# Performance work log

Measured on AMD Instinct MI355X. Metric: run time of the kernel, lower is better.

Reference implementation:

```python
import jax, jax.numpy as jnp
import numpy as np

R, S, C, HID = 8192, 128, 32, 64   # rays, samples/ray, grid_chn, mlp_hidden_chn
G = 128                            # voxel grid resolution
COLOR_CHN = 3
NUM_HARM = 3
OPACITY_INIT_BIAS = -5.0
GAIN = 1.0
HE_DIM = 3 * 2 * NUM_HARM + 3      # harmonic embedding dim = 21

def _relu(x):
    return jnp.maximum(x, 0.0)

def _trilinear(grid, p):
    # grid: [G, G, G, Cg] indexed [z, y, x]; p: [N, 3] xyz coords in [-1, 1]
    g = grid.shape[0]
    c = (p + 1.0) * 0.5 * (g - 1)  # align_corners=True convention
    c0f = jnp.floor(c)
    fr = c - c0f
    c0 = jnp.clip(c0f.astype(jnp.int32), 0, g - 1)
    c1 = jnp.clip(c0 + 1, 0, g - 1)
    x0, y0, z0 = c0[:, 0], c0[:, 1], c0[:, 2]
    x1, y1, z1 = c1[:, 0], c1[:, 1], c1[:, 2]
    fx, fy, fz = fr[:, 0:1], fr[:, 1:2], fr[:, 2:3]
    out = jnp.zeros((p.shape[0], grid.shape[-1]), grid.dtype)
    for xi, wx in ((x0, 1.0 - fx), (x1, fx)):
        for yi, wy in ((y0, 1.0 - fy), (y1, fy)):
            for zi, wz in ((z0, 1.0 - fz), (z1, fz)):
                out = out + (wx * wy * wz) * grid[zi, yi, xi]
    return out

def _harmonic(d):
    # [sin(2^i d), cos(2^i d)] for i<NUM_HARM, with raw direction appended
    freqs = 2.0 ** jnp.arange(NUM_HARM, dtype=jnp.float32)
    ang = d[:, None, :] * freqs[None, :, None]  # [R, NH, 3]
    n = d.shape[0]
    return jnp.concatenate([jnp.sin(ang).reshape(n, -1), jnp.cos(ang).reshape(n, -1), d], axis=-1)

def _forward(origins, directions, near, far, feature_grid, Wr, br, Wt1, bt1, Wt2, bt2, Wo1, bo1, Wo2, bo2, Wc1, bc1, Wc2, bc2):
    n_rays = origins.shape[0]
    # stratified midpoints between near and far
    t = near[:, None] + (far - near)[:, None] * (jnp.arange(S, dtype=jnp.float32) + 0.5) / S
    pts = origins[:, None, :] + t[..., None] * directions[:, None, :]  # [R, S, 3]
    feats = _trilinear(feature_grid, pts.reshape(-1, 3)).reshape(n_rays, S, -1)
    # trunk MLP
    e = _relu(feats @ Wt1 + bt1)
    e = _relu(e @ Wt2 + bt2)
    # opacity MLP (last-layer bias carries opacity_init_bias)
    raw = _relu(e @ Wo1 + bo1) @ Wo2 + bo2  # [R, S, 1]
    density = jax.nn.softplus(GAIN * raw[..., 0])
    delta = ((far - near) / S)[:, None]
    alpha = 1.0 - jnp.exp(-delta * density)  # [R, S]
    trans = jnp.cumprod(1.0 - alpha, axis=1)
    T = jnp.concatenate([jnp.ones((n_rays, 1), alpha.dtype), trans[:, :-1]], axis=1)
    w = T * alpha  # compositing weights
    # color branch: harmonic ray-direction encoding added to color-MLP input
    ray_enc = _harmonic(directions) @ Wr + br  # [R, HID]
    cin = e + ray_enc[:, None, :]
    col = jax.nn.sigmoid(_relu(cin @ Wc1 + bc1) @ Wc2 + bc2)  # [R, S, COLOR_CHN]
    color = jnp.einsum('rs,rsc->rc', w, col)
    mask = 1.0 - trans[:, -1]
    color = color + (1.0 - mask)[:, None] * 0.0  # bg_color = 0.0
    return color, mask

def setup_inputs():
    key = jax.random.key(0)
    ks = jax.random.split(key, 16)
    directions = jax.random.normal(ks[0], (R, 3), jnp.float32)
    directions = directions / jnp.linalg.norm(directions, axis=-1, keepdims=True)
    origins = jnp.zeros((R, 3), jnp.float32)
    near = jnp.full((R,), 0.1, jnp.float32)
    far = jnp.full((R,), 1.0, jnp.float32)
    feature_grid = jax.random.normal(ks[1], (G, G, G, C), jnp.float32) * 0.1
    def lin(k, i, o):
        s = (2.0 / (i + o)) ** 0.5
        return jax.random.normal(k, (i, o), jnp.float32) * s
    return {
        'origins': origins, 'directions': directions, 'near': near, 'far': far,
        'feature_grid': feature_grid,
        'Wr': lin(ks[2], HE_DIM, HID), 'br': jnp.zeros((HID,), jnp.float32),
        'Wt1': lin(ks[3], C, HID), 'bt1': jnp.zeros((HID,), jnp.float32),
        'Wt2': lin(ks[4], HID, HID), 'bt2': jnp.zeros((HID,), jnp.float32),
        'Wo1': lin(ks[5], HID, HID), 'bo1': jnp.zeros((HID,), jnp.float32),
        'Wo2': lin(ks[6], HID, 1), 'bo2': jnp.full((1,), OPACITY_INIT_BIAS, jnp.float32),
        'Wc1': lin(ks[7], HID, HID), 'bc1': jnp.zeros((HID,), jnp.float32),
        'Wc2': lin(ks[8], HID, COLOR_CHN), 'bc2': jnp.zeros((COLOR_CHN,), jnp.float32),
    }

def reference(origins, directions, near, far, feature_grid, Wr, br, Wt1, bt1, Wt2, bt2, Wo1, bo1, Wo2, bo2, Wc1, bc1, Wc2, bc2):
    return _forward(origins, directions, near, far, feature_grid, Wr, br, Wt1, bt1, Wt2, bt2, Wo1, bo1, Wo2, bo2, Wc1, bc1, Wc2, bc2)
```

## Files before the change

### kernel.cpp

```cpp
#include <hip/hip_runtime.h>
#include <math.h>

#define NRAYS 8192
#define XPAD 72

typedef short s16x8 __attribute__((ext_vector_type(8)));
typedef float f32x4 __attribute__((ext_vector_type(4)));

__device__ __forceinline__ unsigned short f2bf(float x){
  unsigned u = __float_as_uint(x);
  u += 0x7FFF + ((u >> 16) & 1);
  return (unsigned short)(u >> 16);
}
__device__ __forceinline__ float bf2f(unsigned short s){ return __uint_as_float(((unsigned)s) << 16); }
__device__ __forceinline__ float softplusf_(float x){ return (x > 20.f) ? x : log1pf(expf(x)); }
__device__ __forceinline__ float sigmoidf_(float x){ return 1.f / (1.f + expf(-x)); }

__global__ void prep_weights(const float* __restrict__ Wt1, const float* __restrict__ Wt2,
                             const float* __restrict__ Wo1, const float* __restrict__ Wc1,
                             unsigned short* __restrict__ ws)
{
  const int i0 = blockIdx.x * blockDim.x + threadIdx.x;
  const int st = gridDim.x * blockDim.x;
  for (int i = i0; i < 2048; i += st){ int n = i >> 5, k = i & 31; ws[i]         = f2bf(Wt1[k * 64 + n]); }
  for (int i = i0; i < 4096; i += st){ int n = i >> 6, k = i & 63; ws[2048 + i]  = f2bf(Wt2[k * 64 + n]); }
  for (int i = i0; i < 4096; i += st){ int n = i >> 6, k = i & 63; ws[6144 + i]  = f2bf(Wo1[k * 64 + n]); }
  for (int i = i0; i < 4096; i += st){ int n = i >> 6, k = i & 63; ws[10240 + i] = f2bf(Wc1[k * 64 + n]); }
}

__device__ __forceinline__ void layer64(const s16x8 a[4][2], const unsigned short* __restrict__ wt,
                                        const float* __restrict__ bias, int ln15, int quad,
                                        f32x4 acc[4][4])
{
  float bv[4];
#pragma unroll
  for (int nt = 0; nt < 4; ++nt) bv[nt] = bias[nt * 16 + ln15];
#pragma unroll
  for (int mt = 0; mt < 4; ++mt)
#pragma unroll
    for (int nt = 0; nt < 4; ++nt){ f32x4 c; c[0] = bv[nt]; c[1] = bv[nt]; c[2] = bv[nt]; c[3] = bv[nt]; acc[mt][nt] = c; }
#pragma unroll
  for (int ks = 0; ks < 2; ++ks){
    s16x8 b[4];
#pragma unroll
    for (int nt = 0; nt < 4; ++nt)
      b[nt] = *(const s16x8*)(wt + (nt * 16 + ln15) * 64 + ks * 32 + quad * 8);
#pragma unroll
    for (int mt = 0; mt < 4; ++mt)
#pragma unroll
      for (int nt = 0; nt < 4; ++nt)
        acc[mt][nt] = __builtin_amdgcn_mfma_f32_16x16x32_bf16(a[mt][ks], b[nt], acc[mt][nt], 0, 0, 0);
  }
}

__device__ __forceinline__ void store_relu(unsigned short* __restrict__ sX, int wrow, int ln15, int quad,
                                           const f32x4 acc[4][4])
{
#pragma unroll
  for (int mt = 0; mt < 4; ++mt){
    const int rowb = wrow + mt * 16 + quad * 4;
#pragma unroll
    for (int nt = 0; nt < 4; ++nt){
      const int col = nt * 16 + ln15;
#pragma unroll
      for (int r = 0; r < 4; ++r)
        sX[(rowb + r) * XPAD + col] = f2bf(fmaxf(acc[mt][nt][r], 0.f));
    }
  }
}

extern "C" __global__ __launch_bounds__(256, 2)
void lightplane_fwd(const float* __restrict__ origins, const float* __restrict__ dirs,
                    const float* __restrict__ nearv,   const float* __restrict__ farv,
                    const float* __restrict__ grid,
                    const float* __restrict__ Wr,  const float* __restrict__ br,
                    const float* __restrict__ bt1, const float* __restrict__ bt2,
                    const float* __restrict__ bo1,
                    const float* __restrict__ Wo2, const float* __restrict__ bo2,
                    const float* __restrict__ bc1,
                    const float* __restrict__ Wc2, const float* __restrict__ bc2,
                    const unsigned short* __restrict__ ws,
                    float* __restrict__ out)
{
  __shared__ unsigned short s_X[256 * XPAD];
  __shared__ float s_scan[2][128];
  __shared__ float s_enc[2][64];
  __shared__ float s_part[2][2][4];

  const int tid   = threadIdx.x;
  const int lane  = tid & 63;
  const int wv    = tid >> 6;
  const int ln15  = lane & 15, quad = lane >> 4;
  const int wrow  = wv * 64;
  const int r_loc = tid >> 7;
  const int s_idx = tid & 127;
  const int ray   = blockIdx.x * 2 + r_loc;

  if (tid < 128) {
    const int rr = tid >> 6, j = tid & 63;
    const int rg = blockIdx.x * 2 + rr;
    const float ddx = dirs[rg * 3 + 0], ddy = dirs[rg * 3 + 1], ddz = dirs[rg * 3 + 2];
    float h[21]; float f = 1.f;
#pragma unroll
    for (int q = 0; q < 3; ++q) {
      h[q * 3 + 0] = sinf(ddx * f); h[q * 3 + 1] = sinf(ddy * f); h[q * 3 + 2] = sinf(ddz * f);
      h[9 + q * 3 + 0] = cosf(ddx * f); h[9 + q * 3 + 1] = cosf(ddy * f); h[9 + q * 3 + 2] = cosf(ddz * f);
      f *= 2.f;
    }
    h[18] = ddx; h[19] = ddy; h[20] = ddz;
    float a = br[j];
#pragma unroll
    for (int i = 0; i < 21; ++i) a = fmaf(h[i], Wr[i * 64 + j], a);
    s_enc[rr][j] = a;
  }

  const float dx = dirs[ray * 3 + 0], dy = dirs[ray * 3 + 1], dz = dirs[ray * 3 + 2];
  const float ox = origins[ray * 3 + 0], oy = origins[ray * 3 + 1], oz = origins[ray * 3 + 2];
  const float nr = nearv[ray], fa = farv[ray];
  const float t  = nr + (fa - nr) * ((s_idx + 0.5f) * (1.0f / 128.0f));
  const float px = fmaf(t, dx, ox), py = fmaf(t, dy, oy), pz = fmaf(t, dz, oz);

  const float cx = (px + 1.f) * 63.5f, cy = (py + 1.f) * 63.5f, cz = (pz + 1.f) * 63.5f;
  const float fx0 = floorf(cx), fy0 = floorf(cy), fz0 = floorf(cz);
  const float frx = cx - fx0, fry = cy - fy0, frz = cz - fz0;
  int ix0 = min(max((int)fx0, 0), 127), iy0 = min(max((int)fy0, 0), 127), iz0 = min(max((int)fz0, 0), 127);
  int ix1 = min(ix0 + 1, 127), iy1 = min(iy0 + 1, 127), iz1 = min(iz0 + 1, 127);
  const float wxs[2] = {1.f - frx, frx}, wys[2] = {1.f - fry, fry}, wzs[2] = {1.f - frz, frz};
  const int xi[2] = {ix0, ix1}, yi[2] = {iy0, iy1}, zi[2] = {iz0, iz1};

  float fe[32];
#pragma unroll
  for (int k = 0; k < 32; ++k) fe[k] = 0.f;
#pragma unroll
  for (int a = 0; a < 2; ++a)
#pragma unroll
    for (int b2 = 0; b2 < 2; ++b2)
#pragma unroll
      for (int c2 = 0; c2 < 2; ++c2) {
        const float wgt = wzs[a] * wys[b2] * wxs[c2];
        const float4* g4 = (const float4*)(grid + ((size_t)((zi[a] * 128 + yi[b2]) * 128 + xi[c2])) * 32);
#pragma unroll
        for (int k = 0; k < 8; ++k) {
          float4 g = g4[k];
          fe[4 * k + 0] = fmaf(wgt, g.x, fe[4 * k + 0]);
          fe[4 * k + 1] = fmaf(wgt, g.y, fe[4 * k + 1]);
          fe[4 * k + 2] = fmaf(wgt, g.z, fe[4 * k + 2]);
          fe[4 * k + 3] = fmaf(wgt, g.w, fe[4 * k + 3]);
        }
      }

#pragma unroll
  for (int q = 0; q < 4; ++q) {
    s16x8 v;
#pragma unroll
    for (int j = 0; j < 8; ++j) v[j] = (short)f2bf(fe[q * 8 + j]);
    *(s16x8*)&s_X[tid * XPAD + q * 8] = v;
  }

  f32x4 acc[4][4];

  {
    s16x8 a1[4];
#pragma unroll
    for (int mt = 0; mt < 4; ++mt)
      a1[mt] = *(const s16x8*)&s_X[(wrow + mt * 16 + ln15) * XPAD + quad * 8];
    float bv[4];
#pragma unroll
    for (int nt = 0; nt < 4; ++nt) bv[nt] = bt1[nt * 16 + ln15];
#pragma unroll
    for (int mt = 0; mt < 4; ++mt)
#pragma unroll
      for (int nt = 0; nt < 4; ++nt){ f32x4 c; c[0]=bv[nt];c[1]=bv[nt];c[2]=bv[nt];c[3]=bv[nt]; acc[mt][nt]=c; }
    s16x8 b[4];
#pragma unroll
    for (int nt = 0; nt < 4; ++nt)
      b[nt] = *(const s16x8*)(ws + (nt * 16 + ln15) * 32 + quad * 8);
#pragma unroll
    for (int mt = 0; mt < 4; ++mt)
#pragma unroll
      for (int nt = 0; nt < 4; ++nt)
        acc[mt][nt] = __builtin_amdgcn_mfma_f32_16x16x32_bf16(a1[mt], b[nt], acc[mt][nt], 0, 0, 0);
    store_relu(s_X, wrow, ln15, quad, acc);
  }

  {
    s16x8 a[4][2];
#pragma unroll
    for (int ks = 0; ks < 2; ++ks)
#pragma unroll
      for (int mt = 0; mt < 4; ++mt)
        a[mt][ks] = *(const s16x8*)&s_X[(wrow + mt * 16 + ln15) * XPAD + ks * 32 + quad * 8];
    layer64(a, ws + 2048, bt2, ln15, quad, acc);
    store_relu(s_X, wrow, ln15, quad, acc);
  }

  s16x8 ea[4][2];
#pragma unroll
  for (int ks = 0; ks < 2; ++ks)
#pragma unroll
    for (int mt = 0; mt < 4; ++mt)
      ea[mt][ks] = *(const s16x8*)&s_X[(wrow + mt * 16 + ln15) * XPAD + ks * 32 + quad * 8];

  layer64(ea, ws + 6144, bo1, ln15, quad, acc);
  store_relu(s_X, wrow, ln15, quad, acc);
  float raw = bo2[0];
#pragma unroll
  for (int q = 0; q < 8; ++q) {
    s16x8 v = *(const s16x8*)&s_X[tid * XPAD + q * 8];
#pragma unroll
    for (int j = 0; j < 8; ++j)
      raw = fmaf(bf2f((unsigned short)v[j]), Wo2[q * 8 + j], raw);
  }
  const float density = softplusf_(raw);
  const float delta   = (fa - nr) * (1.0f / 128.0f);
  const float alpha   = 1.f - expf(-delta * density);

  __syncthreads();

  {
    s16x8 a[4][2];
#pragma unroll
    for (int ks = 0; ks < 2; ++ks) {
      const float* ep = &s_enc[r_loc][ks * 32 + quad * 8];
      float4 e0 = *(const float4*)ep;
      float4 e1 = *(const float4*)(ep + 4);
      float encv[8] = {e0.x, e0.y, e0.z, e0.w, e1.x, e1.y, e1.z, e1.w};
#pragma unroll
      for (int mt = 0; mt < 4; ++mt) {
        s16x8 v;
#pragma unroll
        for (int j = 0; j < 8; ++j)
          v[j] = (short)f2bf(bf2f((unsigned short)ea[mt][ks][j]) + encv[j]);
        a[mt][ks] = v;
      }
    }
    layer64(a, ws + 10240, bc1, ln15, quad, acc);
    store_relu(s_X, wrow, ln15, quad, acc);
  }
  float c0 = bc2[0], c1 = bc2[1], c2 = bc2[2];
#pragma unroll
  for (int q = 0; q < 8; ++q) {
    s16x8 v = *(const s16x8*)&s_X[tid * XPAD + q * 8];
#pragma unroll
    for (int j = 0; j < 8; ++j) {
      const float h = bf2f((unsigned short)v[j]);
      c0 = fmaf(h, Wc2[(q * 8 + j) * 3 + 0], c0);
      c1 = fmaf(h, Wc2[(q * 8 + j) * 3 + 1], c1);
      c2 = fmaf(h, Wc2[(q * 8 + j) * 3 + 2], c2);
    }
  }
  c0 = sigmoidf_(c0); c1 = sigmoidf_(c1); c2 = sigmoidf_(c2);

  float vv = 1.f - alpha;
  s_scan[r_loc][s_idx] = vv;
  __syncthreads();
#pragma unroll
  for (int off = 1; off < 128; off <<= 1) {
    const float u = (s_idx >= off) ? s_scan[r_loc][s_idx - off] : 1.f;
    __syncthreads();
    vv *= u;
    s_scan[r_loc][s_idx] = vv;
    __syncthreads();
  }
  const float Texcl = (s_idx == 0) ? 1.f : s_scan[r_loc][s_idx - 1];
  const float wgt = Texcl * alpha;

  float p0 = wgt * c0, p1 = wgt * c1, p2 = wgt * c2;
#pragma unroll
  for (int off = 32; off > 0; off >>= 1) {
    p0 += __shfl_down(p0, off, 64);
    p1 += __shfl_down(p1, off, 64);
    p2 += __shfl_down(p2, off, 64);
  }
  if ((tid & 63) == 0) {
    const int wvi = s_idx >> 6;
    s_part[r_loc][wvi][0] = p0; s_part[r_loc][wvi][1] = p1; s_part[r_loc][wvi][2] = p2;
  }
  __syncthreads();
  if (s_idx == 0) {
    out[ray * 3 + 0] = s_part[r_loc][0][0] + s_part[r_loc][1][0];
    out[ray * 3 + 1] = s_part[r_loc][0][1] + s_part[r_loc][1][1];
    out[ray * 3 + 2] = s_part[r_loc][0][2] + s_part[r_loc][1][2];
    out[NRAYS * 3 + ray] = 1.f - s_scan[r_loc][127];
  }
}

extern "C" void kernel_launch(void* const* d_in, const int* in_sizes, int n_in,
                              void* d_out, int out_size, void* d_ws, size_t ws_size,
                              hipStream_t stream)
{
  (void)in_sizes; (void)n_in; (void)out_size; (void)ws_size;
  const float* origins = (const float*)d_in[0];
  const float* dirs    = (const float*)d_in[1];
  const float* nearv   = (const float*)d_in[2];
  const float* farv    = (const float*)d_in[3];
  const float* grid    = (const float*)d_in[4];
  const float* Wr  = (const float*)d_in[5];
  const float* br  = (const float*)d_in[6];
  const float* Wt1 = (const float*)d_in[7];
  const float* bt1 = (const float*)d_in[8];
  const float* Wt2 = (const float*)d_in[9];
  const float* bt2 = (const float*)d_in[10];
  const float* Wo1 = (const float*)d_in[11];
  const float* bo1 = (const float*)d_in[12];
  const float* Wo2 = (const float*)d_in[13];
  const float* bo2 = (const float*)d_in[14];
  const float* Wc1 = (const float*)d_in[15];
  const float* bc1 = (const float*)d_in[16];
  const float* Wc2 = (const float*)d_in[17];
  const float* bc2 = (const float*)d_in[18];
  unsigned short* ws = (unsigned short*)d_ws;
  float* out = (float*)d_out;

  prep_weights<<<16, 256, 0, stream>>>(Wt1, Wt2, Wo1, Wc1, ws);
  lightplane_fwd<<<NRAYS / 2, 256, 0, stream>>>(origins, dirs, nearv, farv, grid,
                                                Wr, br, bt1, bt2, bo1, Wo2, bo2,
                                                bc1, Wc2, bc2, ws, out);
}
```

Baseline: 507.9 us.

## Transpose MFMA layout, fuse output heads in registers, use wave-level transmittance scan

The MLP is restructured so the bf16 weights become the MFMA A operand and the per-sample activations become B. Activations stay in small per-wave LDS scratch tiles instead of one shared 256-row buffer. The opacity and color final layers are reduced directly from MFMA accumulators with cross-lane shuffles, which removes the LDS round trips for the last hidden layers. The 128-step block-wide cumulative-product scan, with its many __syncthreads, is replaced by a 64-lane shuffle scan plus a two-wave combine, and launch bounds now allow 4 blocks per SM. In exchange, trunk layer 2 is computed twice (once with the encoding added for the color branch, once without) and register pressure rises under the tighter occupancy bound.

```diff
diff --git a/kernel.cpp b/kernel.cpp
--- a/kernel.cpp
+++ b/kernel.cpp
@@ -1,18 +1,22 @@
 #include <hip/hip_runtime.h>
+#include <hip/hip_bf16.h>
 #include <math.h>
 
 #define NRAYS 8192
-#define XPAD 72
 
 typedef short s16x8 __attribute__((ext_vector_type(8)));
 typedef float f32x4 __attribute__((ext_vector_type(4)));
 
+__device__ __forceinline__ unsigned pk2(float a, float b){
+  union { __hip_bfloat162 h; unsigned u; } cv;
+  cv.h = __float22bfloat162_rn(make_float2(a, b));
+  return cv.u;
+}
 __device__ __forceinline__ unsigned short f2bf(float x){
   unsigned u = __float_as_uint(x);
   u += 0x7FFF + ((u >> 16) & 1);
   return (unsigned short)(u >> 16);
 }
-__device__ __forceinline__ float bf2f(unsigned short s){ return __uint_as_float(((unsigned)s) << 16); }
 __device__ __forceinline__ float softplusf_(float x){ return (x > 20.f) ? x : log1pf(expf(x)); }
 __device__ __forceinline__ float sigmoidf_(float x){ return 1.f / (1.f + expf(-x)); }
 
@@ -28,48 +32,7 @@
   for (int i = i0; i < 4096; i += st){ int n = i >> 6, k = i & 63; ws[10240 + i] = f2bf(Wc1[k * 64 + n]); }
 }
 
-__device__ __forceinline__ void layer64(const s16x8 a[4][2], const unsigned short* __restrict__ wt,
-                                        const float* __restrict__ bias, int ln15, int quad,
-                                        f32x4 acc[4][4])
-{
-  float bv[4];
-#pragma unroll
-  for (int nt = 0; nt < 4; ++nt) bv[nt] = bias[nt * 16 + ln15];
-#pragma unroll
-  for (int mt = 0; mt < 4; ++mt)
-#pragma unroll
-    for (int nt = 0; nt < 4; ++nt){ f32x4 c; c[0] = bv[nt]; c[1] = bv[nt]; c[2] = bv[nt]; c[3] = bv[nt]; acc[mt][nt] = c; }
-#pragma unroll
-  for (int ks = 0; ks < 2; ++ks){
-    s16x8 b[4];
-#pragma unroll
-    for (int nt = 0; nt < 4; ++nt)
-      b[nt] = *(const s16x8*)(wt + (nt * 16 + ln15) * 64 + ks * 32 + quad * 8);
-#pragma unroll
-    for (int mt = 0; mt < 4; ++mt)
-#pragma unroll
-      for (int nt = 0; nt < 4; ++nt)
-        acc[mt][nt] = __builtin_amdgcn_mfma_f32_16x16x32_bf16(a[mt][ks], b[nt], acc[mt][nt], 0, 0, 0);
-  }
-}
-
-__device__ __forceinline__ void store_relu(unsigned short* __restrict__ sX, int wrow, int ln15, int quad,
-                                           const f32x4 acc[4][4])
-{
-#pragma unroll
-  for (int mt = 0; mt < 4; ++mt){
-    const int rowb = wrow + mt * 16 + quad * 4;
-#pragma unroll
-    for (int nt = 0; nt < 4; ++nt){
-      const int col = nt * 16 + ln15;
-#pragma unroll
-      for (int r = 0; r < 4; ++r)
-        sX[(rowb + r) * XPAD + col] = f2bf(fmaxf(acc[mt][nt][r], 0.f));
-    }
-  }
-}
-
-extern "C" __global__ __launch_bounds__(256, 2)
+extern "C" __global__ __launch_bounds__(256, 4)
 void lightplane_fwd(const float* __restrict__ origins, const float* __restrict__ dirs,
                     const float* __restrict__ nearv,   const float* __restrict__ farv,
                     const float* __restrict__ grid,
@@ -82,19 +45,21 @@
                     const unsigned short* __restrict__ ws,
                     float* __restrict__ out)
 {
-  __shared__ unsigned short s_X[256 * XPAD];
-  __shared__ float s_scan[2][128];
+  __shared__ float s_scr[4 * 2304];
   __shared__ float s_enc[2][64];
-  __shared__ float s_part[2][2][4];
-
-  const int tid   = threadIdx.x;
-  const int lane  = tid & 63;
-  const int wv    = tid >> 6;
-  const int ln15  = lane & 15, quad = lane >> 4;
-  const int wrow  = wv * 64;
-  const int r_loc = tid >> 7;
-  const int s_idx = tid & 127;
-  const int ray   = blockIdx.x * 2 + r_loc;
+  __shared__ float s_wtot[2][2];
+  __shared__ float s_part[2][2][3];
+
+  const int tid  = threadIdx.x;
+  const int lane = tid & 63, wv = tid >> 6;
+  const int ln15 = lane & 15, quad = lane >> 4;
+  const int r_loc = wv >> 1, hh = wv & 1;
+  const int ray  = blockIdx.x * 2 + r_loc;
+  const int s_idx = hh * 64 + lane;
+
+  float*          wbase = s_scr + wv * 2304;
+  unsigned*       uscr  = (unsigned*)wbase;
+  unsigned short* fscr  = (unsigned short*)wbase;
 
   if (tid < 128) {
     const int rr = tid >> 6, j = tid & 63;
@@ -134,11 +99,11 @@
 #pragma unroll
   for (int a = 0; a < 2; ++a)
 #pragma unroll
-    for (int b2 = 0; b2 < 2; ++b2)
+    for (int b2i = 0; b2i < 2; ++b2i)
 #pragma unroll
       for (int c2 = 0; c2 < 2; ++c2) {
-        const float wgt = wzs[a] * wys[b2] * wxs[c2];
-        const float4* g4 = (const float4*)(grid + ((size_t)((zi[a] * 128 + yi[b2]) * 128 + xi[c2])) * 32);
+        const float wgt = wzs[a] * wys[b2i] * wxs[c2];
+        const float4* g4 = (const float4*)(grid + ((size_t)((zi[a] * 128 + yi[b2i]) * 128 + xi[c2])) * 32);
 #pragma unroll
         for (int k = 0; k < 8; ++k) {
           float4 g = g4[k];
@@ -149,139 +114,208 @@
         }
       }
 
-#pragma unroll
-  for (int q = 0; q < 4; ++q) {
-    s16x8 v;
-#pragma unroll
-    for (int j = 0; j < 8; ++j) v[j] = (short)f2bf(fe[q * 8 + j]);
-    *(s16x8*)&s_X[tid * XPAD + q * 8] = v;
-  }
-
-  f32x4 acc[4][4];
-
   {
-    s16x8 a1[4];
-#pragma unroll
-    for (int mt = 0; mt < 4; ++mt)
-      a1[mt] = *(const s16x8*)&s_X[(wrow + mt * 16 + ln15) * XPAD + quad * 8];
-    float bv[4];
-#pragma unroll
-    for (int nt = 0; nt < 4; ++nt) bv[nt] = bt1[nt * 16 + ln15];
-#pragma unroll
-    for (int mt = 0; mt < 4; ++mt)
-#pragma unroll
-      for (int nt = 0; nt < 4; ++nt){ f32x4 c; c[0]=bv[nt];c[1]=bv[nt];c[2]=bv[nt];c[3]=bv[nt]; acc[mt][nt]=c; }
-    s16x8 b[4];
-#pragma unroll
-    for (int nt = 0; nt < 4; ++nt)
-      b[nt] = *(const s16x8*)(ws + (nt * 16 + ln15) * 32 + quad * 8);
-#pragma unroll
-    for (int mt = 0; mt < 4; ++mt)
+    unsigned* frow = uscr + lane * 20;
+#pragma unroll
+    for (int q = 0; q < 4; ++q) {
+      uint4 v;
+      v.x = pk2(fe[8 * q + 0], fe[8 * q + 1]); v.y = pk2(fe[8 * q + 2], fe[8 * q + 3]);
+      v.z = pk2(fe[8 * q + 4], fe[8 * q + 5]); v.w = pk2(fe[8 * q + 6], fe[8 * q + 7]);
+      *(uint4*)(frow + 4 * q) = v;
+    }
+  }
+  __syncthreads();
+
+  s16x8 b1[4];
+#pragma unroll
+  for (int nt = 0; nt < 4; ++nt)
+    b1[nt] = *(const s16x8*)(fscr + (16 * nt + ln15) * 40 + quad * 8);
+
+#pragma unroll
+  for (int mt = 0; mt < 4; ++mt) {
+    s16x8 a1 = *(const s16x8*)(ws + (16 * mt + ln15) * 32 + quad * 8);
+    float4 bb = *(const float4*)(bt1 + 16 * mt + 4 * quad);
+    f32x4 acc[4];
+#pragma unroll
+    for (int nt = 0; nt < 4; ++nt) {
+      f32x4 c; c[0] = bb.x; c[1] = bb.y; c[2] = bb.z; c[3] = bb.w;
+      acc[nt] = __builtin_amdgcn_mfma_f32_16x16x32_bf16(a1, b1[nt], c, 0, 0, 0);
+    }
+#pragma unroll
+    for (int nt = 0; nt < 4; ++nt) {
+      uint2 p;
+      p.x = pk2(fmaxf(acc[nt][0], 0.f), fmaxf(acc[nt][1], 0.f));
+      p.y = pk2(fmaxf(acc[nt][2], 0.f), fmaxf(acc[nt][3], 0.f));
+      *(uint2*)(uscr + (16 * nt + ln15) * 36 + 8 * mt + 2 * quad) = p;
+    }
+  }
+  s16x8 b2[4][2];
+#pragma unroll
+  for (int nt = 0; nt < 4; ++nt)
+#pragma unroll
+    for (int ks = 0; ks < 2; ++ks)
+      b2[nt][ks] = *(const s16x8*)(uscr + (16 * nt + ln15) * 36 + 16 * ks + 4 * quad);
+
+#pragma unroll
+  for (int mt = 0; mt < 4; ++mt) {
+    float4 bb = *(const float4*)(bt2 + 16 * mt + 4 * quad);
+    f32x4 acc[4];
+#pragma unroll
+    for (int nt = 0; nt < 4; ++nt) { f32x4 c; c[0]=bb.x;c[1]=bb.y;c[2]=bb.z;c[3]=bb.w; acc[nt]=c; }
+#pragma unroll
+    for (int ks = 0; ks < 2; ++ks) {
+      s16x8 a = *(const s16x8*)(ws + 2048 + (16 * mt + ln15) * 64 + ks * 32 + quad * 8);
 #pragma unroll
       for (int nt = 0; nt < 4; ++nt)
-        acc[mt][nt] = __builtin_amdgcn_mfma_f32_16x16x32_bf16(a1[mt], b[nt], acc[mt][nt], 0, 0, 0);
-    store_relu(s_X, wrow, ln15, quad, acc);
-  }
-
-  {
-    s16x8 a[4][2];
+        acc[nt] = __builtin_amdgcn_mfma_f32_16x16x32_bf16(a, b2[nt][ks], acc[nt], 0, 0, 0);
+    }
+    float4 en = *(const float4*)(&s_enc[r_loc][16 * mt + 4 * quad]);
+#pragma unroll
+    for (int nt = 0; nt < 4; ++nt) {
+      uint2 p;
+      p.x = pk2(fmaxf(acc[nt][0], 0.f) + en.x, fmaxf(acc[nt][1], 0.f) + en.y);
+      p.y = pk2(fmaxf(acc[nt][2], 0.f) + en.z, fmaxf(acc[nt][3], 0.f) + en.w);
+      *(uint2*)(uscr + (16 * nt + ln15) * 36 + 8 * mt + 2 * quad) = p;
+    }
+  }
+  s16x8 b4[4][2];
+#pragma unroll
+  for (int nt = 0; nt < 4; ++nt)
 #pragma unroll
     for (int ks = 0; ks < 2; ++ks)
-#pragma unroll
-      for (int mt = 0; mt < 4; ++mt)
-        a[mt][ks] = *(const s16x8*)&s_X[(wrow + mt * 16 + ln15) * XPAD + ks * 32 + quad * 8];
-    layer64(a, ws + 2048, bt2, ln15, quad, acc);
-    store_relu(s_X, wrow, ln15, quad, acc);
-  }
-
-  s16x8 ea[4][2];
-#pragma unroll
-  for (int ks = 0; ks < 2; ++ks)
-#pragma unroll
-    for (int mt = 0; mt < 4; ++mt)
-      ea[mt][ks] = *(const s16x8*)&s_X[(wrow + mt * 16 + ln15) * XPAD + ks * 32 + quad * 8];
-
-  layer64(ea, ws + 6144, bo1, ln15, quad, acc);
-  store_relu(s_X, wrow, ln15, quad, acc);
-  float raw = bo2[0];
-#pragma unroll
-  for (int q = 0; q < 8; ++q) {
-    s16x8 v = *(const s16x8*)&s_X[tid * XPAD + q * 8];
-#pragma unroll
-    for (int j = 0; j < 8; ++j)
-      raw = fmaf(bf2f((unsigned short)v[j]), Wo2[q * 8 + j], raw);
-  }
-  const float density = softplusf_(raw);
-  const float delta   = (fa - nr) * (1.0f / 128.0f);
-  const float alpha   = 1.f - expf(-delta * density);
-
+      b4[nt][ks] = *(const s16x8*)(uscr + (16 * nt + ln15) * 36 + 16 * ks + 4 * quad);
+
+#pragma unroll
+  for (int mt = 0; mt < 4; ++mt) {
+    float4 bb = *(const float4*)(bt2 + 16 * mt + 4 * quad);
+    f32x4 acc[4];
+#pragma unroll
+    for (int nt = 0; nt < 4; ++nt) { f32x4 c; c[0]=bb.x;c[1]=bb.y;c[2]=bb.z;c[3]=bb.w; acc[nt]=c; }
+#pragma unroll
+    for (int ks = 0; ks < 2; ++ks) {
+      s16x8 a = *(const s16x8*)(ws + 2048 + (16 * mt + ln15) * 64 + ks * 32 + quad * 8);
+#pragma unroll
+      for (int nt = 0; nt < 4; ++nt)
+        acc[nt] = __builtin_amdgcn_mfma_f32_16x16x32_bf16(a, b2[nt][ks], acc[nt], 0, 0, 0);
+    }
+#pragma unroll
+    for (int nt = 0; nt < 4; ++nt) {
+      uint2 p;
+      p.x = pk2(fmaxf(acc[nt][0], 0.f), fmaxf(acc[nt][1], 0.f));
+      p.y = pk2(fmaxf(acc[nt][2], 0.f), fmaxf(acc[nt][3], 0.f));
+      *(uint2*)(uscr + (16 * nt + ln15) * 36 + 8 * mt + 2 * quad) = p;
+    }
+  }
+  s16x8 b3[4][2];
+#pragma unroll
+  for (int nt = 0; nt < 4; ++nt)
+#pragma unroll
+    for (int ks = 0; ks < 2; ++ks)
+      b3[nt][ks] = *(const s16x8*)(uscr + (16 * nt + ln15) * 36 + 16 * ks + 4 * quad);
+
+  float p_o[4] = {0.f, 0.f, 0.f, 0.f};
+  float pc0[4] = {0.f, 0.f, 0.f, 0.f}, pc1[4] = {0.f, 0.f, 0.f, 0.f}, pc2[4] = {0.f, 0.f, 0.f, 0.f};
+#pragma unroll
+  for (int mt = 0; mt < 4; ++mt) {
+    {
+      float4 bb = *(const float4*)(bo1 + 16 * mt + 4 * quad);
+      f32x4 acc[4];
+#pragma unroll
+      for (int nt = 0; nt < 4; ++nt) { f32x4 c; c[0]=bb.x;c[1]=bb.y;c[2]=bb.z;c[3]=bb.w; acc[nt]=c; }
+#pragma unroll
+      for (int ks = 0; ks < 2; ++ks) {
+        s16x8 a = *(const s16x8*)(ws + 6144 + (16 * mt + ln15) * 64 + ks * 32 + quad * 8);
+#pragma unroll
+        for (int nt = 0; nt < 4; ++nt)
+          acc[nt] = __builtin_amdgcn_mfma_f32_16x16x32_bf16(a, b3[nt][ks], acc[nt], 0, 0, 0);
+      }
+      float4 wo = *(const float4*)(Wo2 + 16 * mt + 4 * quad);
+#pragma unroll
+      for (int nt = 0; nt < 4; ++nt)
+        p_o[nt] += fmaxf(acc[nt][0], 0.f) * wo.x + fmaxf(acc[nt][1], 0.f) * wo.y +
+                   fmaxf(acc[nt][2], 0.f) * wo.z + fmaxf(acc[nt][3], 0.f) * wo.w;
+    }
+    {
+      float4 bb = *(const float4*)(bc1 + 16 * mt + 4 * quad);
+      f32x4 acc[4];
+#pragma unroll
+      for (int nt = 0; nt < 4; ++nt) { f32x4 c; c[0]=bb.x;c[1]=bb.y;c[2]=bb.z;c[3]=bb.w; acc[nt]=c; }
+#pragma unroll
+      for (int ks = 0; ks < 2; ++ks) {
+        s16x8 a = *(const s16x8*)(ws + 10240 + (16 * mt + ln15) * 64 + ks * 32 + quad * 8);
+#pragma unroll
+        for (int nt = 0; nt < 4; ++nt)
+          acc[nt] = __builtin_amdgcn_mfma_f32_16x16x32_bf16(a, b4[nt][ks], acc[nt], 0, 0, 0);
+      }
+      float wcf[12];
+      const float* wc = Wc2 + (16 * mt + 4 * quad) * 3;
+      *(float4*)&wcf[0] = ((const float4*)wc)[0];
+      *(float4*)&wcf[4] = ((const float4*)wc)[1];
+      *(float4*)&wcf[8] = ((const float4*)wc)[2];
+#pragma unroll
+      for (int nt = 0; nt < 4; ++nt)
+#pragma unroll
+        for (int r = 0; r < 4; ++r) {
+          const float hv = fmaxf(acc[nt][r], 0.f);
+          pc0[nt] = fmaf(hv, wcf[r * 3 + 0], pc0[nt]);
+          pc1[nt] = fmaf(hv, wcf[r * 3 + 1], pc1[nt]);
+          pc2[nt] = fmaf(hv, wcf[r * 3 + 2], pc2[nt]);
+        }
+    }
+  }
+#pragma unroll
+  for (int nt = 0; nt < 4; ++nt) {
+    p_o[nt] += __shfl_xor(p_o[nt], 16, 64); p_o[nt] += __shfl_xor(p_o[nt], 32, 64);
+    pc0[nt] += __shfl_xor(pc0[nt], 16, 64); pc0[nt] += __shfl_xor(pc0[nt], 32, 64);
+    pc1[nt] += __shfl_xor(pc1[nt], 16, 64); pc1[nt] += __shfl_xor(pc1[nt], 32, 64);
+    pc2[nt] += __shfl_xor(pc2[nt], 16, 64); pc2[nt] += __shfl_xor(pc2[nt], 32, 64);
+  }
+
+  const float delta = (fa - nr) * (1.0f / 128.0f);
+  const float bo2v = bo2[0], bc2x = bc2[0], bc2y = bc2[1], bc2z = bc2[2];
+  float A_[4], C0[4], C1[4], C2[4];
+#pragma unroll
+  for (int nt = 0; nt < 4; ++nt) {
+    const float dens = softplusf_(p_o[nt] + bo2v);
+    A_[nt] = 1.f - expf(-delta * dens);
+    C0[nt] = sigmoidf_(pc0[nt] + bc2x);
+    C1[nt] = sigmoidf_(pc1[nt] + bc2y);
+    C2[nt] = sigmoidf_(pc2[nt] + bc2z);
+  }
+  const float a_own = (quad < 2) ? (quad == 0 ? A_[0] : A_[1]) : (quad == 2 ? A_[2] : A_[3]);
+  const float c0own = (quad < 2) ? (quad == 0 ? C0[0] : C0[1]) : (quad == 2 ? C0[2] : C0[3]);
+  const float c1own = (quad < 2) ? (quad == 0 ? C1[0] : C1[1]) : (quad == 2 ? C1[2] : C1[3]);
+  const float c2own = (quad < 2) ? (quad == 0 ? C2[0] : C2[1]) : (quad == 2 ? C2[2] : C2[3]);
+
+  float v = 1.f - a_own;
+#pragma unroll
+  for (int off = 1; off < 64; off <<= 1) {
+    const float u = __shfl_up(v, off, 64);
+    if (lane >= off) v *= u;
+  }
+  const float tot = __shfl(v, 63, 64);
+  if (lane == 0) s_wtot[r_loc][hh] = tot;
+  float excl = __shfl_up(v, 1, 64);
+  if (lane == 0) excl = 1.f;
   __syncthreads();
-
-  {
-    s16x8 a[4][2];
-#pragma unroll
-    for (int ks = 0; ks < 2; ++ks) {
-      const float* ep = &s_enc[r_loc][ks * 32 + quad * 8];
-      float4 e0 = *(const float4*)ep;
-      float4 e1 = *(const float4*)(ep + 4);
-      float encv[8] = {e0.x, e0.y, e0.z, e0.w, e1.x, e1.y, e1.z, e1.w};
-#pragma unroll
-      for (int mt = 0; mt < 4; ++mt) {
-        s16x8 v;
-#pragma unroll
-        for (int j = 0; j < 8; ++j)
-          v[j] = (short)f2bf(bf2f((unsigned short)ea[mt][ks][j]) + encv[j]);
-        a[mt][ks] = v;
-      }
-    }
-    layer64(a, ws + 10240, bc1, ln15, quad, acc);
-    store_relu(s_X, wrow, ln15, quad, acc);
-  }
-  float c0 = bc2[0], c1 = bc2[1], c2 = bc2[2];
-#pragma unroll
-  for (int q = 0; q < 8; ++q) {
-    s16x8 v = *(const s16x8*)&s_X[tid * XPAD + q * 8];
-#pragma unroll
-    for (int j = 0; j < 8; ++j) {
-      const float h = bf2f((unsigned short)v[j]);
-      c0 = fmaf(h, Wc2[(q * 8 + j) * 3 + 0], c0);
-      c1 = fmaf(h, Wc2[(q * 8 + j) * 3 + 1], c1);
-      c2 = fmaf(h, Wc2[(q * 8 + j) * 3 + 2], c2);
-    }
-  }
-  c0 = sigmoidf_(c0); c1 = sigmoidf_(c1); c2 = sigmoidf_(c2);
-
-  float vv = 1.f - alpha;
-  s_scan[r_loc][s_idx] = vv;
-  __syncthreads();
-#pragma unroll
-  for (int off = 1; off < 128; off <<= 1) {
-    const float u = (s_idx >= off) ? s_scan[r_loc][s_idx - off] : 1.f;
-    __syncthreads();
-    vv *= u;
-    s_scan[r_loc][s_idx] = vv;
-    __syncthreads();
-  }
-  const float Texcl = (s_idx == 0) ? 1.f : s_scan[r_loc][s_idx - 1];
-  const float wgt = Texcl * alpha;
-
-  float p0 = wgt * c0, p1 = wgt * c1, p2 = wgt * c2;
+  const float prefix = hh ? s_wtot[r_loc][0] : 1.f;
+  const float Ttot   = s_wtot[r_loc][0] * s_wtot[r_loc][1];
+  const float wgt = prefix * excl * a_own;
+
+  float p0 = wgt * c0own, p1 = wgt * c1own, p2 = wgt * c2own;
 #pragma unroll
   for (int off = 32; off > 0; off >>= 1) {
     p0 += __shfl_down(p0, off, 64);
     p1 += __shfl_down(p1, off, 64);
     p2 += __shfl_down(p2, off, 64);
   }
-  if ((tid & 63) == 0) {
-    const int wvi = s_idx >> 6;
-    s_part[r_loc][wvi][0] = p0; s_part[r_loc][wvi][1] = p1; s_part[r_loc][wvi][2] = p2;
-  }
+  if (lane == 0) { s_part[r_loc][hh][0] = p0; s_part[r_loc][hh][1] = p1; s_part[r_loc][hh][2] = p2; }
   __syncthreads();
-  if (s_idx == 0) {
+  if (hh == 0 && lane == 0) {
     out[ray * 3 + 0] = s_part[r_loc][0][0] + s_part[r_loc][1][0];
     out[ray * 3 + 1] = s_part[r_loc][0][1] + s_part[r_loc][1][1];
     out[ray * 3 + 2] = s_part[r_loc][0][2] + s_part[r_loc][1][2];
-    out[NRAYS * 3 + ray] = 1.f - s_scan[r_loc][127];
+    out[NRAYS * 3 + ray] = 1.f - Ttot;
   }
 }
 
```

New measurement: 591.4 us. 1.16x slower.
